# Performance work log

Hardware: AMD Instinct MI355X
Metric: run time of the kernel (lower is better)

Reference implementation:

```python
import jax, jax.numpy as jnp
import numpy as np

DIM = 512
NUM_HEADS = 4
SCALE = 1.0 / np.sqrt(DIM)  # note: module scales by 1/sqrt(dim), not 1/sqrt(head_dim)


def setup_inputs() -> dict:
    key = jax.random.key(0)
    k1, k2, k3, k4, k5, k6 = jax.random.split(key, 6)
    B, N, M, C = 8, 2048, 2048, DIM
    bound = 1.0 / np.sqrt(C)
    return {
        "F1": jax.random.normal(k1, (B, N, C), dtype=jnp.float32),
        "F2": jax.random.normal(k2, (B, M, C), dtype=jnp.float32),
        "W_qkv": jax.random.uniform(k3, (C, C), jnp.float32, -bound, bound),
        "b_qkv": jax.random.uniform(k4, (C,), jnp.float32, -bound, bound),
        "W_proj": jax.random.uniform(k5, (C, C), jnp.float32, -bound, bound),
        "b_proj": jax.random.uniform(k6, (C,), jnp.float32, -bound, bound),
    }


def reference(F1, F2, W_qkv, b_qkv, W_proj, b_proj):
    B, N, C = F1.shape
    M = F2.shape[1]
    H, D = NUM_HEADS, C // NUM_HEADS
    # shared qkv projection (same weights for q, k and v in the original module)
    q = (F1 @ W_qkv + b_qkv).reshape(B, N, H, D)  # queries from F1
    kv = (F2 @ W_qkv + b_qkv).reshape(B, M, H, D)  # keys == values from F2
    attn = jnp.einsum("bnhd,bmhd->bhnm", q * SCALE, kv)
    attn = jax.nn.softmax(attn, axis=-1)
    x = jnp.einsum("bhnm,bmhd->bnhd", attn, kv).reshape(B, N, C)
    return x @ W_proj + b_proj
```

## Files before the change

### kernel.cpp

```cpp
#include <hip/hip_runtime.h>
#include <math.h>


typedef __attribute__((ext_vector_type(8))) short s16x8;
typedef __attribute__((ext_vector_type(4))) float f32x4;

#define C_DIM 512
#define HDIM  128
#define NROWS 16384
#define SCALE_Q 0.04419417382415922f
#define LOG2E   1.4426950408889634f

__device__ __forceinline__ unsigned short f2bf(float f) {
    union { float f; unsigned u; } v; v.f = f;
    unsigned r = v.u + 0x7fffu + ((v.u >> 16) & 1u);
    return (unsigned short)(r >> 16);
}

__device__ __forceinline__ void async16(const void* g, void* l) {
    __builtin_amdgcn_global_load_lds(
        (const __attribute__((address_space(1))) void*)g,
        (__attribute__((address_space(3))) void*)l, 16, 0, 0);
}

__global__ __launch_bounds__(256)
void conv_bf16_2(const float* __restrict__ s0, const float* __restrict__ s1,
                 unsigned short* __restrict__ d0, unsigned short* __restrict__ d1,
                 int n8) {
    const float* src = blockIdx.y ? s1 : s0;
    unsigned short* dst = blockIdx.y ? d1 : d0;
    int i = blockIdx.x * 256 + threadIdx.x;
    if (i >= n8) return;
    float4 a = ((const float4*)src)[2 * i];
    float4 b = ((const float4*)src)[2 * i + 1];
    union { unsigned short us[8]; uint4 v; } o;
    o.us[0] = f2bf(a.x); o.us[1] = f2bf(a.y); o.us[2] = f2bf(a.z); o.us[3] = f2bf(a.w);
    o.us[4] = f2bf(b.x); o.us[5] = f2bf(b.y); o.us[6] = f2bf(b.z); o.us[7] = f2bf(b.w);
    ((uint4*)dst)[i] = o.v;
}

__global__ __launch_bounds__(256)
void wconv_t2(const float* __restrict__ W0, const float* __restrict__ W1,
              unsigned short* __restrict__ T0, unsigned short* __restrict__ T1) {
    const float* W = blockIdx.z ? W1 : W0;
    unsigned short* Wt = blockIdx.z ? T1 : T0;
    __shared__ float t[64][65];
    const int k0 = blockIdx.y * 64, n0 = blockIdx.x * 64;
    const int c = threadIdx.x & 63, r0 = threadIdx.x >> 6;
#pragma unroll
    for (int r = r0; r < 64; r += 4)
        t[r][c] = W[(size_t)(k0 + r) * C_DIM + n0 + c];
    __syncthreads();
#pragma unroll
    for (int r = r0; r < 64; r += 4)
        Wt[(size_t)(n0 + r) * C_DIM + k0 + c] = f2bf(t[c][r]);
}

template <int OUT_BF16>
__global__ __launch_bounds__(256, 3)
void gemm_bt(const unsigned short* __restrict__ A,
             const unsigned short* __restrict__ Bt,
             const float* __restrict__ bias,
             void* __restrict__ Cv, float oscTop, int topRows) {
    __shared__ __align__(16) unsigned short As[128][64];
    __shared__ __align__(16) unsigned short Bs[128][64];

    const int tid  = threadIdx.x;
    const int wid  = tid >> 6;
    const int lane = tid & 63;
    const int lr   = lane & 15;
    const int quad = lane >> 4;
    const int wm   = wid >> 1;
    const int wn   = wid & 1;
    const int rowBase = blockIdx.y * 128;
    const int colBase = blockIdx.x * 128;
    const int srow = lane >> 3;
    const int soff = srow * C_DIM + (((lane & 7) ^ (srow & 7)) * 8);
    const float osc = (rowBase < topRows) ? oscTop : 1.0f;

    f32x4 acc[4][4];
#pragma unroll
    for (int i = 0; i < 4; i++)
#pragma unroll
        for (int j = 0; j < 4; j++) acc[i][j] = (f32x4)0.0f;

    for (int kt = 0; kt < 8; kt++) {
        const int k0 = kt * 64;
        __syncthreads();
#pragma unroll
        for (int i = 0; i < 4; i++) {
            const int R = wid * 32 + i * 8;
            async16(A  + (size_t)(rowBase + R) * C_DIM + k0 + soff, &As[R][0]);
            async16(Bt + (size_t)(colBase + R) * C_DIM + k0 + soff, &Bs[R][0]);
        }
        __syncthreads();

#pragma unroll
        for (int s = 0; s < 2; s++) {
            s16x8 af[4], bf[4];
#pragma unroll
            for (int i = 0; i < 4; i++)
                af[i] = *(const s16x8*)&As[wm * 64 + i * 16 + lr][((s * 4 + quad) ^ (lr & 7)) * 8];
#pragma unroll
            for (int j = 0; j < 4; j++)
                bf[j] = *(const s16x8*)&Bs[wn * 64 + j * 16 + lr][((s * 4 + quad) ^ (lr & 7)) * 8];
#pragma unroll
            for (int i = 0; i < 4; i++)
#pragma unroll
                for (int j = 0; j < 4; j++)
                    acc[i][j] = __builtin_amdgcn_mfma_f32_16x16x32_bf16(af[i], bf[j], acc[i][j], 0, 0, 0);
        }
    }

    float bcol[4];
#pragma unroll
    for (int j = 0; j < 4; j++)
        bcol[j] = bias[colBase + wn * 64 + j * 16 + lr];
#pragma unroll
    for (int i = 0; i < 4; i++) {
#pragma unroll
        for (int j = 0; j < 4; j++) {
            const int col = colBase + wn * 64 + j * 16 + lr;
#pragma unroll
            for (int r = 0; r < 4; r++) {
                const int row = rowBase + wm * 64 + i * 16 + quad * 4 + r;
                float v = (acc[i][j][r] + bcol[j]) * osc;
                if (OUT_BF16)
                    ((unsigned short*)Cv)[(size_t)row * C_DIM + col] = f2bf(v);
                else
                    ((float*)Cv)[(size_t)row * C_DIM + col] = v;
            }
        }
    }
}

__global__ __launch_bounds__(256, 3)
void cross_attn(const unsigned short* __restrict__ Q,
                const unsigned short* __restrict__ KV,
                unsigned short* __restrict__ X) {
    __shared__ __align__(16) unsigned short Kt[64][128];
    __shared__ __align__(16) unsigned short Vt[128][72];
    __shared__ __align__(16) unsigned short Pl[4][32][72];

    const int tid  = threadIdx.x;
    const int wid  = tid >> 6;
    const int lane = tid & 63;
    const int lr   = lane & 15;
    const int quad = lane >> 4;
    const int b    = blockIdx.z;
    const int h    = blockIdx.y;
    const int hoff = h * HDIM;
    const int kap  = lr * 4 + quad;
    const int l7   = lane & 7;
    const size_t qrow0  = (size_t)b * 2048 + blockIdx.x * 128 + wid * 32;
    const size_t kvrow0 = (size_t)b * 2048;

    s16x8 qf[2][4];
#pragma unroll
    for (int i = 0; i < 2; i++)
#pragma unroll
        for (int kk = 0; kk < 4; kk++)
            qf[i][kk] = *(const s16x8*)(Q + (qrow0 + i * 16 + lr) * C_DIM + hoff + kk * 32 + quad * 8);

    f32x4 O[2][8];
#pragma unroll
    for (int i = 0; i < 2; i++)
#pragma unroll
        for (int dt = 0; dt < 8; dt++) O[i][dt] = (f32x4)0.0f;
    float lacc[2][4];
#pragma unroll
    for (int i = 0; i < 2; i++)
#pragma unroll
        for (int r = 0; r < 4; r++) lacc[i][r] = 0.0f;

    for (int kt = 0; kt < 32; kt++) {
        const int key0 = kt * 64;
        __syncthreads();
#pragma unroll
        for (int i = 0; i < 4; i++) {
            const int dc = wid + 4 * i;
            uint4 v = *(const uint4*)(KV + (kvrow0 + key0 + kap) * C_DIM + hoff + dc * 8);
            *(uint4*)&Kt[lane][(dc ^ l7) * 8] = v;
            const unsigned short* e = (const unsigned short*)&v;
#pragma unroll
            for (int t = 0; t < 8; t++) Vt[dc * 8 + t][kap] = e[t];
        }
        __syncthreads();

        f32x4 s[2][4];
#pragma unroll
        for (int i = 0; i < 2; i++)
#pragma unroll
            for (int j = 0; j < 4; j++) s[i][j] = (f32x4)0.0f;
#pragma unroll
        for (int kk = 0; kk < 4; kk++) {
#pragma unroll
            for (int j = 0; j < 4; j++) {
                s16x8 kf = *(const s16x8*)&Kt[j * 16 + lr][((kk * 4 + quad) ^ (lr & 7)) * 8];
                s[0][j] = __builtin_amdgcn_mfma_f32_16x16x32_bf16(qf[0][kk], kf, s[0][j], 0, 0, 0);
                s[1][j] = __builtin_amdgcn_mfma_f32_16x16x32_bf16(qf[1][kk], kf, s[1][j], 0, 0, 0);
            }
        }

#pragma unroll
        for (int i = 0; i < 2; i++) {
#pragma unroll
            for (int r = 0; r < 4; r++) {
                float p0 = exp2f(s[i][0][r]);
                float p1 = exp2f(s[i][1][r]);
                float p2 = exp2f(s[i][2][r]);
                float p3 = exp2f(s[i][3][r]);
                lacc[i][r] += (p0 + p1) + (p2 + p3);
                uint2 pk;
                pk.x = (unsigned)f2bf(p0) | ((unsigned)f2bf(p1) << 16);
                pk.y = (unsigned)f2bf(p2) | ((unsigned)f2bf(p3) << 16);
                *(uint2*)&Pl[wid][i * 16 + quad * 4 + r][4 * lr] = pk;
            }
        }

#pragma unroll
        for (int kk = 0; kk < 2; kk++) {
            s16x8 pa0 = *(const s16x8*)&Pl[wid][lr][kk * 32 + quad * 8];
            s16x8 pa1 = *(const s16x8*)&Pl[wid][16 + lr][kk * 32 + quad * 8];
#pragma unroll
            for (int dt = 0; dt < 8; dt++) {
                s16x8 vf = *(const s16x8*)&Vt[dt * 16 + lr][kk * 32 + quad * 8];
                O[0][dt] = __builtin_amdgcn_mfma_f32_16x16x32_bf16(pa0, vf, O[0][dt], 0, 0, 0);
                O[1][dt] = __builtin_amdgcn_mfma_f32_16x16x32_bf16(pa1, vf, O[1][dt], 0, 0, 0);
            }
        }
    }

#pragma unroll
    for (int i = 0; i < 2; i++) {
#pragma unroll
        for (int r = 0; r < 4; r++) {
            float l = lacc[i][r];
#pragma unroll
            for (int off = 1; off < 16; off <<= 1)
                l += __shfl_xor(l, off);
            const float inv = 1.0f / l;
            const size_t row = (qrow0 + i * 16 + quad * 4 + r) * C_DIM + hoff;
#pragma unroll
            for (int dt = 0; dt < 8; dt++)
                X[row + dt * 16 + lr] = f2bf(O[i][dt][r] * inv);
        }
    }
}

extern "C" void kernel_launch(void* const* d_in, const int* in_sizes, int n_in,
                              void* d_out, int out_size, void* d_ws, size_t ws_size,
                              hipStream_t stream) {
    const float* F1     = (const float*)d_in[0];
    const float* F2     = (const float*)d_in[1];
    const float* W_qkv  = (const float*)d_in[2];
    const float* b_qkv  = (const float*)d_in[3];
    const float* W_proj = (const float*)d_in[4];
    const float* b_proj = (const float*)d_in[5];
    float* out = (float*)d_out;

    const size_t NC = (size_t)NROWS * C_DIM;
    unsigned short* F1b = (unsigned short*)d_ws;
    unsigned short* F2b = F1b + NC;
    unsigned short* Qw  = F2b + NC;
    unsigned short* KVw = Qw  + NC;
    unsigned short* Wqt = KVw + NC;
    unsigned short* Wpt = Wqt + C_DIM * C_DIM;
    unsigned short* Xw  = F1b;

    dim3 blk(256);

    conv_bf16_2<<<dim3(NC / 8 / 256, 2), blk, 0, stream>>>(F1, F2, F1b, F2b, (int)(NC / 8));
    wconv_t2<<<dim3(8, 8, 2), blk, 0, stream>>>(W_qkv, W_proj, Wqt, Wpt);

    gemm_bt<1><<<dim3(4, 256), blk, 0, stream>>>(F1b, Wqt, b_qkv, Qw, SCALE_Q * LOG2E, NROWS);
    cross_attn<<<dim3(16, 4, 8), blk, 0, stream>>>(Qw, KVw, Xw);
    gemm_bt<0><<<dim3(4, 128), blk, 0, stream>>>(Xw, Wpt, b_proj, out, 1.0f, 0);
}
```

Before: 282.5 us.

## Fuse fp32->bf16 input conversion into QKV GEMM and emit transposed KV for attention

Result: slower. 322.9 us (+14.3%).

```diff
diff --git a/kernel.cpp b/kernel.cpp
--- a/kernel.cpp
+++ b/kernel.cpp
@@ -21,22 +21,6 @@
     __builtin_amdgcn_global_load_lds(
         (const __attribute__((address_space(1))) void*)g,
         (__attribute__((address_space(3))) void*)l, 16, 0, 0);
-}
-
-__global__ __launch_bounds__(256)
-void conv_bf16_2(const float* __restrict__ s0, const float* __restrict__ s1,
-                 unsigned short* __restrict__ d0, unsigned short* __restrict__ d1,
-                 int n8) {
-    const float* src = blockIdx.y ? s1 : s0;
-    unsigned short* dst = blockIdx.y ? d1 : d0;
-    int i = blockIdx.x * 256 + threadIdx.x;
-    if (i >= n8) return;
-    float4 a = ((const float4*)src)[2 * i];
-    float4 b = ((const float4*)src)[2 * i + 1];
-    union { unsigned short us[8]; uint4 v; } o;
-    o.us[0] = f2bf(a.x); o.us[1] = f2bf(a.y); o.us[2] = f2bf(a.z); o.us[3] = f2bf(a.w);
-    o.us[4] = f2bf(b.x); o.us[5] = f2bf(b.y); o.us[6] = f2bf(b.z); o.us[7] = f2bf(b.w);
-    ((uint4*)dst)[i] = o.v;
 }
 
 __global__ __launch_bounds__(256)
@@ -56,12 +40,14 @@
         Wt[(size_t)(n0 + r) * C_DIM + k0 + c] = f2bf(t[c][r]);
 }
 
-template <int OUT_BF16>
+template <int A_FP32, int WRITE_KVT, int OUT_BF16>
 __global__ __launch_bounds__(256, 3)
-void gemm_bt(const unsigned short* __restrict__ A,
+void gemm_bt(const unsigned short* __restrict__ Abf,
+             const float* __restrict__ Af1, const float* __restrict__ Af2,
              const unsigned short* __restrict__ Bt,
              const float* __restrict__ bias,
-             void* __restrict__ Cv, float oscTop, int topRows) {
+             void* __restrict__ Cv, unsigned short* __restrict__ KVt,
+             float oscTop, int topRows) {
     __shared__ __align__(16) unsigned short As[128][64];
     __shared__ __align__(16) unsigned short Bs[128][64];
 
@@ -77,6 +63,9 @@
     const int srow = lane >> 3;
     const int soff = srow * C_DIM + (((lane & 7) ^ (srow & 7)) * 8);
     const float osc = (rowBase < topRows) ? oscTop : 1.0f;
+    const float* Afp = (A_FP32 && rowBase < topRows)
+                           ? (Af1 + (size_t)rowBase * C_DIM)
+                           : (Af2 + (size_t)(rowBase - topRows) * C_DIM);
 
     f32x4 acc[4][4];
 #pragma unroll
@@ -87,10 +76,32 @@
     for (int kt = 0; kt < 8; kt++) {
         const int k0 = kt * 64;
         __syncthreads();
+        if (A_FP32) {
+#pragma unroll
+            for (int i = 0; i < 4; i++) {
+                const int chunkid = tid + 256 * i;
+                const int row = chunkid >> 3, c = chunkid & 7;
+                const int pos = c ^ (row & 7);
+                const float* p = Afp + (size_t)row * C_DIM + k0 + c * 8;
+                float4 v0 = *(const float4*)p;
+                float4 v1 = *(const float4*)(p + 4);
+                union { unsigned short us[8]; uint4 v; } o;
+                o.us[0] = f2bf(v0.x); o.us[1] = f2bf(v0.y);
+                o.us[2] = f2bf(v0.z); o.us[3] = f2bf(v0.w);
+                o.us[4] = f2bf(v1.x); o.us[5] = f2bf(v1.y);
+                o.us[6] = f2bf(v1.z); o.us[7] = f2bf(v1.w);
+                *(uint4*)&As[row][pos * 8] = o.v;
+            }
+        } else {
+#pragma unroll
+            for (int i = 0; i < 4; i++) {
+                const int R = wid * 32 + i * 8;
+                async16(Abf + (size_t)(rowBase + R) * C_DIM + k0 + soff, &As[R][0]);
+            }
+        }
 #pragma unroll
         for (int i = 0; i < 4; i++) {
             const int R = wid * 32 + i * 8;
-            async16(A  + (size_t)(rowBase + R) * C_DIM + k0 + soff, &As[R][0]);
             async16(Bt + (size_t)(colBase + R) * C_DIM + k0 + soff, &Bs[R][0]);
         }
         __syncthreads();
@@ -112,6 +123,10 @@
         }
     }
 
+    const int isKV = WRITE_KVT && (rowBase >= topRows);
+    const int rk0  = rowBase - topRows;
+    const int bKV  = (rk0 >> 11);
+    const int keyB = (rk0 & 2047) + wm * 64 + quad * 4;
     float bcol[4];
 #pragma unroll
     for (int j = 0; j < 4; j++)
@@ -121,14 +136,28 @@
 #pragma unroll
         for (int j = 0; j < 4; j++) {
             const int col = colBase + wn * 64 + j * 16 + lr;
-#pragma unroll
-            for (int r = 0; r < 4; r++) {
-                const int row = rowBase + wm * 64 + i * 16 + quad * 4 + r;
-                float v = (acc[i][j][r] + bcol[j]) * osc;
-                if (OUT_BF16)
-                    ((unsigned short*)Cv)[(size_t)row * C_DIM + col] = f2bf(v);
-                else
-                    ((float*)Cv)[(size_t)row * C_DIM + col] = v;
+            const int row = rowBase + wm * 64 + i * 16 + quad * 4;
+            float v[4];
+#pragma unroll
+            for (int r = 0; r < 4; r++)
+                v[r] = (acc[i][j][r] + bcol[j]) * osc;
+            if (OUT_BF16) {
+                unsigned short* Cb = (unsigned short*)Cv;
+#pragma unroll
+                for (int r = 0; r < 4; r++)
+                    Cb[(size_t)(row + r) * C_DIM + col] = f2bf(v[r]);
+            } else {
+                float* Cf = (float*)Cv;
+#pragma unroll
+                for (int r = 0; r < 4; r++)
+                    Cf[(size_t)(row + r) * C_DIM + col] = v[r];
+            }
+            if (isKV) {
+                const int h = col >> 7, d = col & 127;
+                uint2 pk;
+                pk.x = (unsigned)f2bf(v[0]) | ((unsigned)f2bf(v[1]) << 16);
+                pk.y = (unsigned)f2bf(v[2]) | ((unsigned)f2bf(v[3]) << 16);
+                *(uint2*)&KVt[((size_t)(bKV * 4 + h) * 128 + d) * 2048 + keyB + i * 16] = pk;
             }
         }
     }
@@ -137,9 +166,10 @@
 __global__ __launch_bounds__(256, 3)
 void cross_attn(const unsigned short* __restrict__ Q,
                 const unsigned short* __restrict__ KV,
+                const unsigned short* __restrict__ KVt,
                 unsigned short* __restrict__ X) {
     __shared__ __align__(16) unsigned short Kt[64][128];
-    __shared__ __align__(16) unsigned short Vt[128][72];
+    __shared__ __align__(16) unsigned short Vt[128][64];
     __shared__ __align__(16) unsigned short Pl[4][32][72];
 
     const int tid  = threadIdx.x;
@@ -150,10 +180,14 @@
     const int b    = blockIdx.z;
     const int h    = blockIdx.y;
     const int hoff = h * HDIM;
-    const int kap  = lr * 4 + quad;
-    const int l7   = lane & 7;
     const size_t qrow0  = (size_t)b * 2048 + blockIdx.x * 128 + wid * 32;
     const size_t kvrow0 = (size_t)b * 2048;
+    const unsigned short* KVtbh = KVt + ((size_t)(b * 4 + h) * 128) * 2048;
+
+    const int ktR   = lane >> 4;
+    const int ktp   = lane & 15;
+    const int vtR   = lane >> 3;
+    const int vtp   = lane & 7;
 
     s16x8 qf[2][4];
 #pragma unroll
@@ -178,12 +212,18 @@
         __syncthreads();
 #pragma unroll
         for (int i = 0; i < 4; i++) {
-            const int dc = wid + 4 * i;
-            uint4 v = *(const uint4*)(KV + (kvrow0 + key0 + kap) * C_DIM + hoff + dc * 8);
-            *(uint4*)&Kt[lane][(dc ^ l7) * 8] = v;
-            const unsigned short* e = (const unsigned short*)&v;
-#pragma unroll
-            for (int t = 0; t < 8; t++) Vt[dc * 8 + t][kap] = e[t];
+            const int Rb = (wid * 4 + i) * 4;
+            const int R  = Rb + ktR;
+            const int kapR = 4 * (R & 15) + (R >> 4);
+            const int sc = (ktp & 8) | ((ktp & 7) ^ (R & 7));
+            async16(KV + (kvrow0 + key0 + kapR) * C_DIM + hoff + sc * 8, &Kt[Rb][0]);
+        }
+#pragma unroll
+        for (int i = 0; i < 4; i++) {
+            const int Rb = (wid * 4 + i) * 8;
+            const int R  = Rb + vtR;
+            const int c  = vtp ^ (R & 7);
+            async16(KVtbh + (size_t)R * 2048 + key0 + c * 8, &Vt[Rb][0]);
         }
         __syncthreads();
 
@@ -224,7 +264,7 @@
             s16x8 pa1 = *(const s16x8*)&Pl[wid][16 + lr][kk * 32 + quad * 8];
 #pragma unroll
             for (int dt = 0; dt < 8; dt++) {
-                s16x8 vf = *(const s16x8*)&Vt[dt * 16 + lr][kk * 32 + quad * 8];
+                s16x8 vf = *(const s16x8*)&Vt[dt * 16 + lr][((kk * 4 + quad) ^ (lr & 7)) * 8];
                 O[0][dt] = __builtin_amdgcn_mfma_f32_16x16x32_bf16(pa0, vf, O[0][dt], 0, 0, 0);
                 O[1][dt] = __builtin_amdgcn_mfma_f32_16x16x32_bf16(pa1, vf, O[1][dt], 0, 0, 0);
             }
@@ -260,20 +300,20 @@
     float* out = (float*)d_out;
 
     const size_t NC = (size_t)NROWS * C_DIM;
-    unsigned short* F1b = (unsigned short*)d_ws;
-    unsigned short* F2b = F1b + NC;
-    unsigned short* Qw  = F2b + NC;
+    unsigned short* Qw  = (unsigned short*)d_ws;
     unsigned short* KVw = Qw  + NC;
-    unsigned short* Wqt = KVw + NC;
+    unsigned short* KVt = KVw + NC;
+    unsigned short* Xw  = KVt + NC;
+    unsigned short* Wqt = Xw  + NC;
     unsigned short* Wpt = Wqt + C_DIM * C_DIM;
-    unsigned short* Xw  = F1b;
 
     dim3 blk(256);
 
-    conv_bf16_2<<<dim3(NC / 8 / 256, 2), blk, 0, stream>>>(F1, F2, F1b, F2b, (int)(NC / 8));
     wconv_t2<<<dim3(8, 8, 2), blk, 0, stream>>>(W_qkv, W_proj, Wqt, Wpt);
 
-    gemm_bt<1><<<dim3(4, 256), blk, 0, stream>>>(F1b, Wqt, b_qkv, Qw, SCALE_Q * LOG2E, NROWS);
-    cross_attn<<<dim3(16, 4, 8), blk, 0, stream>>>(Qw, KVw, Xw);
-    gemm_bt<0><<<dim3(4, 128), blk, 0, stream>>>(Xw, Wpt, b_proj, out, 1.0f, 0);
-}
+    gemm_bt<1, 1, 1><<<dim3(4, 256), blk, 0, stream>>>(
+        nullptr, F1, F2, Wqt, b_qkv, Qw, KVt, SCALE_Q * LOG2E, NROWS);
+    cross_attn<<<dim3(16, 4, 8), blk, 0, stream>>>(Qw, KVw, KVt, Xw);
+    gemm_bt<0, 0, 0><<<dim3(4, 128), blk, 0, stream>>>(
+        Xw, nullptr, nullptr, Wpt, b_proj, out, nullptr, 1.0f, 0);
+}
```
